# Performance work log

Hardware: AMD Instinct MI355X
Metric: run time of the kernel (lower is better)

## Reference

```python
import jax, jax.numpy as jnp
import numpy as np

ALPHA = 0.25
GAMMA = 2.0
CLS_EPS = 1e-4


def _make_boxes(key, n, img=512.0, smin=32.0, smax=128.0, yx=False):
    k1, k2, k3, k4 = jax.random.split(key, 4)
    cx = jax.random.uniform(k1, (n,)) * img
    cy = jax.random.uniform(k2, (n,)) * img
    w = smin + jax.random.uniform(k3, (n,)) * (smax - smin)
    h = smin + jax.random.uniform(k4, (n,)) * (smax - smin)
    if yx:  # anchor format (y1, x1, y2, x2)
        return jnp.stack([cy - h / 2, cx - w / 2, cy + h / 2, cx + w / 2], axis=1)
    # annotation format (x1, y1, x2, y2)
    return jnp.stack([cx - w / 2, cy - h / 2, cx + w / 2, cy + h / 2], axis=1)


def setup_inputs() -> dict:
    key = jax.random.key(0)
    B, A, C, M = 4, 100000, 80, 32
    k = jax.random.split(key, 6)
    classifications = jax.random.uniform(k[0], (B, A, C), dtype=jnp.float32)
    regressions = jax.random.normal(k[1], (B, A, 7), dtype=jnp.float32)
    anchors = _make_boxes(k[2], A, yx=True)[None]  # [1, A, 4] (y1,x1,y2,x2)
    boxes = jax.vmap(lambda kk: _make_boxes(kk, M))(jax.random.split(k[3], B))  # [B, M, 4]
    labels = jax.random.randint(k[4], (B, M), 0, C).astype(jnp.float32)
    annotations = jnp.concatenate([boxes, labels[..., None]], axis=-1)  # [B, M, 5]
    return {"classifications": classifications, "regressions": regressions,
            "anchors": anchors, "annotations": annotations}


def reference(classifications, regressions, anchors, annotations):
    B, A, C = classifications.shape
    anchor = anchors[0]  # [A, 4] (y1, x1, y2, x2)
    aw = anchor[:, 3] - anchor[:, 1]
    ah = anchor[:, 2] - anchor[:, 0]
    acx = anchor[:, 1] + 0.5 * aw
    acy = anchor[:, 0] + 0.5 * ah
    area_a = (anchor[:, 2] - anchor[:, 0]) * (anchor[:, 3] - anchor[:, 1])

    def per_image(cls, reg, ann):
        M_ = ann.shape[0]
        b = ann[:, :4]  # (x1, y1, x2, y2)
        labels = ann[:, 4].astype(jnp.int32)
        cls = jnp.clip(cls, CLS_EPS, 1.0 - CLS_EPS)
        # IoU [A, M] (same axis convention as calc_iou)
        iw = jnp.clip(jnp.minimum(anchor[:, 3:4], b[None, :, 2]) - jnp.maximum(anchor[:, 1:2], b[None, :, 0]), 0.0)
        ih = jnp.clip(jnp.minimum(anchor[:, 2:3], b[None, :, 3]) - jnp.maximum(anchor[:, 0:1], b[None, :, 1]), 0.0)
        area_b = (b[:, 2] - b[:, 0]) * (b[:, 3] - b[:, 1])
        inter = iw * ih
        ua = jnp.clip(area_a[:, None] + area_b[None, :] - inter, 1e-8)
        iou = inter / ua
        iou_max = iou.max(axis=1)
        iou_argmax = iou.argmax(axis=1)  # [A]
        pos = iou_max >= 0.5
        neg = iou_max < 0.4
        num_pos = pos.sum()
        posf = pos.astype(cls.dtype)
        # classification targets: -1 ignore, 0 background, one-hot positives
        assigned_box = b[iou_argmax]           # [A, 4]
        assigned_lbl = labels[iou_argmax]      # [A]
        onehot = jax.nn.one_hot(assigned_lbl, C, dtype=cls.dtype)
        tgt = jnp.where(pos[:, None], onehot, jnp.where(neg[:, None], 0.0, -1.0))
        alpha_f = jnp.where(tgt == 1.0, ALPHA, 1.0 - ALPHA)
        focal_w = alpha_f * jnp.where(tgt == 1.0, 1.0 - cls, cls) ** GAMMA
        bce = -(tgt * jnp.log(cls) + (1.0 - tgt) * jnp.log(1.0 - cls))
        cls_loss = jnp.where(tgt != -1.0, focal_w * bce, 0.0).sum() / jnp.maximum(num_pos.astype(cls.dtype), 1.0)
        gw = assigned_box[:, 2] - assigned_box[:, 0]
        gh = assigned_box[:, 3] - assigned_box[:, 1]
        gcx = assigned_box[:, 0] + 0.5 * gw
        gcy = assigned_box[:, 1] + 0.5 * gh
        gw = jnp.clip(gw, 1.0)
        gh = jnp.clip(gh, 1.0)
        rt = jnp.stack([(gcy - acy) / ah, (gcx - acx) / aw,
                        jnp.log(gh / ah), jnp.log(gw / aw)], axis=1)  # [A, 4] (dy,dx,dh,dw)
        diff = jnp.abs(rt - reg[:, :4])
        sl1 = jnp.where(diff <= 1.0 / 9.0, 0.5 * 9.0 * diff ** 2, diff - 0.5 / 9.0)
        reg_loss = (sl1 * posf[:, None]).sum() / jnp.maximum(num_pos * 4, 1).astype(cls.dtype)
        # embedding grouping loss (segment mean per GT box over positive anchors)
        emb = reg[:, 4:7]
        counts = jax.ops.segment_sum(posf, iou_argmax, num_segments=M_)          # [M]
        sums = jax.ops.segment_sum(emb * posf[:, None], iou_argmax, num_segments=M_)  # [M, 3]
        mean = jnp.where((counts > 0)[:, None], sums / jnp.maximum(counts, 1.0)[:, None], 0.0)
        mdet = jax.lax.stop_gradient(mean)
        sq = jax.ops.segment_sum((((emb - mdet[iou_argmax]) ** 2).sum(-1)) * posf, iou_argmax, num_segments=M_)
        per_ann = jnp.where(counts > 0, sq / jnp.maximum(counts * 3.0, 1.0), 0.0)
        emb_loss = per_ann.sum() / M_
        return cls_loss, reg_loss, emb_loss, mean

    cls_l, reg_l, emb_l, embs = jax.vmap(per_image)(classifications, regressions, annotations)
    losses = jnp.stack([cls_l.mean(), reg_l.mean() * 50.0, emb_l.mean()])
    return losses, embs
```

## Files before the change

### kernel.cpp

```cpp
#include <hip/hip_runtime.h>

#define CLS_LO 1.0e-4f
#define CLS_HI 0.9999f


__device__ __forceinline__ float smooth_l1(float d) {
    d = fabsf(d);
    return (d <= (1.0f / 9.0f)) ? (4.5f * d * d) : (d - (0.5f / 9.0f));
}

__global__ void __launch_bounds__(256)
det_main_kernel(const float* __restrict__ cls,
                const float* __restrict__ reg,
                const float* __restrict__ anc,
                const float* __restrict__ ann,
                float* __restrict__ ws,
                int A, int C, int M, int NB)
{
    const int b   = blockIdx.y;
    const int tid = threadIdx.x;
    const int a0  = blockIdx.x * 256;
    const int a   = a0 + tid;
    const int S   = 5 * M + 3 * NB;

    __shared__ float sb[5 * 64];
    __shared__ float s_cnt[64], s_sx[64], s_sy[64], s_sz[64], s_sq[64];
    __shared__ float s_maskf[256];

    for (int i = tid; i < M * 5; i += 256)
        sb[i] = ann[(size_t)b * M * 5 + i];
    if (tid < M) { s_cnt[tid] = 0.f; s_sx[tid] = 0.f; s_sy[tid] = 0.f; s_sz[tid] = 0.f; s_sq[tid] = 0.f; }
    s_maskf[tid] = 0.f;
    __syncthreads();

    float contrib_cls = 0.f, contrib_reg = 0.f, contrib_np = 0.f;

    if (a < A) {
        float4 av = ((const float4*)anc)[a];
        const float ay1 = av.x, ax1 = av.y, ay2 = av.z, ax2 = av.w;
        const float aw  = ax2 - ax1;
        const float ah  = ay2 - ay1;
        const float acx = ax1 + 0.5f * aw;
        const float acy = ay1 + 0.5f * ah;
        const float area_a = ah * aw;

        float best = -1.0f;
        int   bj   = 0;
#define IOU_BODY(j)                                                              \
        {                                                                        \
            const float bx1 = sb[(j) * 5 + 0];                                   \
            const float by1 = sb[(j) * 5 + 1];                                   \
            const float bx2 = sb[(j) * 5 + 2];                                   \
            const float by2 = sb[(j) * 5 + 3];                                   \
            float iw = fminf(ax2, bx2) - fmaxf(ax1, bx1); iw = fmaxf(iw, 0.f);   \
            float ih = fminf(ay2, by2) - fmaxf(ay1, by1); ih = fmaxf(ih, 0.f);   \
            const float inter = iw * ih;                                         \
            const float ua = fmaxf(area_a + (bx2 - bx1) * (by2 - by1) - inter,   \
                                   1e-8f);                                       \
            const float iou = inter / ua;                                        \
            if (iou > best) { best = iou; bj = (j); }                            \
        }
        if (M == 32) {
            #pragma unroll
            for (int j = 0; j < 32; j++) IOU_BODY(j)
        } else {
            for (int j = 0; j < M; j++) IOU_BODY(j)
        }
#undef IOU_BODY
        const bool pos = best >= 0.5f;
        const bool neg = best < 0.4f;
        s_maskf[tid] = (pos || neg) ? 1.0f : 0.0f;

        if (pos) {
            contrib_np = 1.0f;

            const float* cbase = cls + ((size_t)b * A + a) * (size_t)C;
            const int L = (int)sb[bj * 5 + 4];
            const float p = fminf(fmaxf(cbase[L], CLS_LO), CLS_HI);
            contrib_cls = 0.25f * (1.f - p) * (1.f - p) * (-__logf(p))
                        - 0.75f * p * p * (-__logf(1.f - p));

            const float* rp = reg + ((size_t)b * A + a) * 7;
            const float r0 = rp[0], r1 = rp[1], r2 = rp[2], r3 = rp[3];
            const float e0 = rp[4], e1 = rp[5], e2 = rp[6];

            const float bx1 = sb[bj * 5 + 0];
            const float by1 = sb[bj * 5 + 1];
            const float bx2 = sb[bj * 5 + 2];
            const float by2 = sb[bj * 5 + 3];
            float gw = bx2 - bx1;
            float gh = by2 - by1;
            const float gcx = bx1 + 0.5f * gw;
            const float gcy = by1 + 0.5f * gh;
            gw = fmaxf(gw, 1.f);
            gh = fmaxf(gh, 1.f);
            contrib_reg = smooth_l1((gcy - acy) / ah - r0) +
                          smooth_l1((gcx - acx) / aw - r1) +
                          smooth_l1(logf(gh / ah) - r2) +
                          smooth_l1(logf(gw / aw) - r3);

            atomicAdd(&s_cnt[bj], 1.f);
            atomicAdd(&s_sx[bj], e0);
            atomicAdd(&s_sy[bj], e1);
            atomicAdd(&s_sz[bj], e2);
            atomicAdd(&s_sq[bj], e0 * e0 + e1 * e1 + e2 * e2);
        }
    }
    __syncthreads();

    {
        const float4* tile = (const float4*)(cls + ((size_t)b * A + a0) * (size_t)C);
        float acc = 0.f;
        if (a0 + 256 <= A && C == 80) {
            #pragma unroll 5
            for (int k = 0; k < 20; k++) {
                const int e4 = tid + 256 * k;
                const float m = s_maskf[(unsigned)e4 / 20u];
                const float4 v = tile[e4];
                float p, l, s = 0.f;
                p = fminf(fmaxf(v.x, CLS_LO), CLS_HI); l = __logf(1.f - p); s = fmaf(p * p, l, s);
                p = fminf(fmaxf(v.y, CLS_LO), CLS_HI); l = __logf(1.f - p); s = fmaf(p * p, l, s);
                p = fminf(fmaxf(v.z, CLS_LO), CLS_HI); l = __logf(1.f - p); s = fmaf(p * p, l, s);
                p = fminf(fmaxf(v.w, CLS_LO), CLS_HI); l = __logf(1.f - p); s = fmaf(p * p, l, s);
                acc = fmaf(m, s, acc);
            }
        } else {
            const int nA   = min(256, A - a0);
            const int cpa4 = C >> 2;
            const int n4   = nA * cpa4;
            for (int e4 = tid; e4 < n4; e4 += 256) {
                const float m = s_maskf[(unsigned)e4 / (unsigned)cpa4];
                const float4 v = tile[e4];
                float p, l, s = 0.f;
                p = fminf(fmaxf(v.x, CLS_LO), CLS_HI); l = __logf(1.f - p); s = fmaf(p * p, l, s);
                p = fminf(fmaxf(v.y, CLS_LO), CLS_HI); l = __logf(1.f - p); s = fmaf(p * p, l, s);
                p = fminf(fmaxf(v.z, CLS_LO), CLS_HI); l = __logf(1.f - p); s = fmaf(p * p, l, s);
                p = fminf(fmaxf(v.w, CLS_LO), CLS_HI); l = __logf(1.f - p); s = fmaf(p * p, l, s);
                acc = fmaf(m, s, acc);
            }
        }
        contrib_cls -= 0.75f * acc;
    }

    for (int off = 32; off > 0; off >>= 1) {
        contrib_cls += __shfl_down(contrib_cls, off, 64);
        contrib_reg += __shfl_down(contrib_reg, off, 64);
        contrib_np  += __shfl_down(contrib_np,  off, 64);
    }
    __shared__ float s_part[4][3];
    if ((tid & 63) == 0) {
        s_part[tid >> 6][0] = contrib_cls;
        s_part[tid >> 6][1] = contrib_reg;
        s_part[tid >> 6][2] = contrib_np;
    }
    __syncthreads();

    float* wsb = ws + (size_t)b * S;
    if (tid < M) {
        const float c = s_cnt[tid];
        if (c != 0.f) {
            atomicAdd(&wsb[tid], c);
            atomicAdd(&wsb[M + 3 * tid + 0], s_sx[tid]);
            atomicAdd(&wsb[M + 3 * tid + 1], s_sy[tid]);
            atomicAdd(&wsb[M + 3 * tid + 2], s_sz[tid]);
            atomicAdd(&wsb[4 * M + tid], s_sq[tid]);
        }
    }
    if (tid == 0) {
        float* slot = wsb + 5 * M + 3 * blockIdx.x;
        slot[0] = s_part[0][0] + s_part[1][0] + s_part[2][0] + s_part[3][0];
        slot[1] = s_part[0][1] + s_part[1][1] + s_part[2][1] + s_part[3][1];
        slot[2] = s_part[0][2] + s_part[1][2] + s_part[2][2] + s_part[3][2];
    }
}

__global__ void __launch_bounds__(256)
det_final_kernel(const float* __restrict__ ws,
                 float* __restrict__ out,
                 int B, int M, int NB)
{
    const int t = threadIdx.x;
    const int S = 5 * M + 3 * NB;
    __shared__ float s_scal[8][3];
    __shared__ float s_emb[8];
    __shared__ float tmp[4][3];
    if (t < B) s_emb[t] = 0.f;

    for (int b = 0; b < B; b++) {
        const float* slots = ws + (size_t)b * S + 5 * M;
        float c = 0.f, r = 0.f, n = 0.f;
        for (int i = t; i < NB; i += 256) {
            c += slots[3 * i + 0];
            r += slots[3 * i + 1];
            n += slots[3 * i + 2];
        }
        for (int off = 32; off > 0; off >>= 1) {
            c += __shfl_down(c, off, 64);
            r += __shfl_down(r, off, 64);
            n += __shfl_down(n, off, 64);
        }
        if ((t & 63) == 0) { tmp[t >> 6][0] = c; tmp[t >> 6][1] = r; tmp[t >> 6][2] = n; }
        __syncthreads();
        if (t == 0) {
            s_scal[b][0] = tmp[0][0] + tmp[1][0] + tmp[2][0] + tmp[3][0];
            s_scal[b][1] = tmp[0][1] + tmp[1][1] + tmp[2][1] + tmp[3][1];
            s_scal[b][2] = tmp[0][2] + tmp[1][2] + tmp[2][2] + tmp[3][2];
        }
        __syncthreads();
    }

    if (t < B * M) {
        const int b = t / M;
        const int m = t - b * M;
        const float* wsb = ws + (size_t)b * S;
        const float c = wsb[m];
        float mx = 0.f, my = 0.f, mz = 0.f, pa = 0.f;
        if (c > 0.f) {
            mx = wsb[M + 3 * m + 0] / c;
            my = wsb[M + 3 * m + 1] / c;
            mz = wsb[M + 3 * m + 2] / c;
            const float sq = wsb[4 * M + m] - c * (mx * mx + my * my + mz * mz);
            pa = sq / fmaxf(c * 3.f, 1.f);
        }
        out[3 + (size_t)(b * M + m) * 3 + 0] = mx;
        out[3 + (size_t)(b * M + m) * 3 + 1] = my;
        out[3 + (size_t)(b * M + m) * 3 + 2] = mz;
        atomicAdd(&s_emb[b], pa);
    }
    __syncthreads();

    if (t == 0) {
        float cl = 0.f, rl = 0.f, el = 0.f;
        for (int b = 0; b < B; b++) {
            const float np = s_scal[b][2];
            cl += s_scal[b][0] / fmaxf(np, 1.f);
            rl += s_scal[b][1] / fmaxf(4.f * np, 1.f);
            el += s_emb[b] / (float)M;
        }
        const float invB = 1.f / (float)B;
        out[0] = cl * invB;
        out[1] = rl * invB * 50.f;
        out[2] = el * invB;
    }
}

extern "C" void kernel_launch(void* const* d_in, const int* in_sizes, int n_in,
                              void* d_out, int out_size, void* d_ws, size_t ws_size,
                              hipStream_t stream) {
    const float* cls = (const float*)d_in[0];
    const float* reg = (const float*)d_in[1];
    const float* anc = (const float*)d_in[2];
    const float* ann = (const float*)d_in[3];
    float* out = (float*)d_out;
    float* ws  = (float*)d_ws;

    const int A = in_sizes[2] / 4;
    const int B = in_sizes[1] / (A * 7);
    const int C = in_sizes[0] / (B * A);
    const int M = in_sizes[3] / (B * 5);
    const int NB = (A + 255) / 256;
    const int S  = 5 * M + 3 * NB;

    hipMemsetAsync(ws, 0, (size_t)B * S * sizeof(float), stream);

    dim3 grid(NB, B);
    det_main_kernel<<<grid, 256, 0, stream>>>(cls, reg, anc, ann, ws, A, C, M, NB);
    det_final_kernel<<<1, 256, 0, stream>>>(ws, out, B, M, NB);
}
```

Measured before the change: 224.9 us.

## Split IoU assignment and focal-loss streaming into separate kernels with byte mask

Splits the fused kernel in two. An assignment kernel computes IoU, writes a per-anchor byte mask to workspace and accumulates the positive-anchor terms. A focal kernel then streams the classification tensor in 64-anchor blocks, using a multiply-shift in place of the division for the mask index. Block partials are now folded into 64 atomic slots per image, so the final reduction is a single wavefront shuffle. This aims to separate the ALU-heavy IoU phase from the bandwidth-bound streaming phase and to raise the block count for the bandwidth phase, at the cost of an extra launch and mask traffic.

```diff
diff --git a/kernel.cpp b/kernel.cpp
--- a/kernel.cpp
+++ b/kernel.cpp
@@ -10,27 +10,30 @@
 }
 
 __global__ void __launch_bounds__(256)
-det_main_kernel(const float* __restrict__ cls,
-                const float* __restrict__ reg,
-                const float* __restrict__ anc,
-                const float* __restrict__ ann,
-                float* __restrict__ ws,
-                int A, int C, int M, int NB)
+det_assign_kernel(const float* __restrict__ cls,
+                  const float* __restrict__ reg,
+                  const float* __restrict__ anc,
+                  const float* __restrict__ ann,
+                  float* __restrict__ ws,
+                  unsigned char* __restrict__ mask,
+                  int A, int C, int M)
 {
     const int b   = blockIdx.y;
     const int tid = threadIdx.x;
-    const int a0  = blockIdx.x * 256;
-    const int a   = a0 + tid;
-    const int S   = 5 * M + 3 * NB;
-
-    __shared__ float sb[5 * 64];
-    __shared__ float s_cnt[64], s_sx[64], s_sy[64], s_sz[64], s_sq[64];
-    __shared__ float s_maskf[256];
-
-    for (int i = tid; i < M * 5; i += 256)
-        sb[i] = ann[(size_t)b * M * 5 + i];
-    if (tid < M) { s_cnt[tid] = 0.f; s_sx[tid] = 0.f; s_sy[tid] = 0.f; s_sz[tid] = 0.f; s_sq[tid] = 0.f; }
-    s_maskf[tid] = 0.f;
+    const int a   = blockIdx.x * 256 + tid;
+    const int S   = 5 * M + 192;
+
+    __shared__ float4 sbox[64];
+    __shared__ float  slbl[64];
+    __shared__ float  s_cnt[64], s_sx[64], s_sy[64], s_sz[64], s_sq[64];
+    __shared__ float  s_part[4][3];
+
+    if (tid < M) {
+        const float* bp = ann + ((size_t)b * M + tid) * 5;
+        sbox[tid] = make_float4(bp[0], bp[1], bp[2], bp[3]);
+        slbl[tid] = bp[4];
+        s_cnt[tid] = 0.f; s_sx[tid] = 0.f; s_sy[tid] = 0.f; s_sz[tid] = 0.f; s_sq[tid] = 0.f;
+    }
     __syncthreads();
 
     float contrib_cls = 0.f, contrib_reg = 0.f, contrib_np = 0.f;
@@ -40,23 +43,18 @@
         const float ay1 = av.x, ax1 = av.y, ay2 = av.z, ax2 = av.w;
         const float aw  = ax2 - ax1;
         const float ah  = ay2 - ay1;
-        const float acx = ax1 + 0.5f * aw;
-        const float acy = ay1 + 0.5f * ah;
         const float area_a = ah * aw;
 
         float best = -1.0f;
         int   bj   = 0;
 #define IOU_BODY(j)                                                              \
         {                                                                        \
-            const float bx1 = sb[(j) * 5 + 0];                                   \
-            const float by1 = sb[(j) * 5 + 1];                                   \
-            const float bx2 = sb[(j) * 5 + 2];                                   \
-            const float by2 = sb[(j) * 5 + 3];                                   \
-            float iw = fminf(ax2, bx2) - fmaxf(ax1, bx1); iw = fmaxf(iw, 0.f);   \
-            float ih = fminf(ay2, by2) - fmaxf(ay1, by1); ih = fmaxf(ih, 0.f);   \
+            const float4 bx = sbox[(j)];                                         \
+            float iw = fminf(ax2, bx.z) - fmaxf(ax1, bx.x); iw = fmaxf(iw, 0.f); \
+            float ih = fminf(ay2, bx.w) - fmaxf(ay1, bx.y); ih = fmaxf(ih, 0.f); \
             const float inter = iw * ih;                                         \
-            const float ua = fmaxf(area_a + (bx2 - bx1) * (by2 - by1) - inter,   \
-                                   1e-8f);                                       \
+            const float ua = fmaxf(area_a + (bx.z - bx.x) * (bx.w - bx.y)        \
+                                   - inter, 1e-8f);                              \
             const float iou = inter / ua;                                        \
             if (iou > best) { best = iou; bj = (j); }                            \
         }
@@ -69,13 +67,13 @@
 #undef IOU_BODY
         const bool pos = best >= 0.5f;
         const bool neg = best < 0.4f;
-        s_maskf[tid] = (pos || neg) ? 1.0f : 0.0f;
+        mask[(size_t)b * A + a] = (pos || neg) ? 1 : 0;
 
         if (pos) {
             contrib_np = 1.0f;
 
             const float* cbase = cls + ((size_t)b * A + a) * (size_t)C;
-            const int L = (int)sb[bj * 5 + 4];
+            const int L = (int)slbl[bj];
             const float p = fminf(fmaxf(cbase[L], CLS_LO), CLS_HI);
             contrib_cls = 0.25f * (1.f - p) * (1.f - p) * (-__logf(p))
                         - 0.75f * p * p * (-__logf(1.f - p));
@@ -84,16 +82,15 @@
             const float r0 = rp[0], r1 = rp[1], r2 = rp[2], r3 = rp[3];
             const float e0 = rp[4], e1 = rp[5], e2 = rp[6];
 
-            const float bx1 = sb[bj * 5 + 0];
-            const float by1 = sb[bj * 5 + 1];
-            const float bx2 = sb[bj * 5 + 2];
-            const float by2 = sb[bj * 5 + 3];
-            float gw = bx2 - bx1;
-            float gh = by2 - by1;
-            const float gcx = bx1 + 0.5f * gw;
-            const float gcy = by1 + 0.5f * gh;
+            const float4 bx = sbox[bj];
+            float gw = bx.z - bx.x;
+            float gh = bx.w - bx.y;
+            const float gcx = bx.x + 0.5f * gw;
+            const float gcy = bx.y + 0.5f * gh;
             gw = fmaxf(gw, 1.f);
             gh = fmaxf(gh, 1.f);
+            const float acx = ax1 + 0.5f * aw;
+            const float acy = ay1 + 0.5f * ah;
             contrib_reg = smooth_l1((gcy - acy) / ah - r0) +
                           smooth_l1((gcx - acx) / aw - r1) +
                           smooth_l1(logf(gh / ah) - r2) +
@@ -106,48 +103,12 @@
             atomicAdd(&s_sq[bj], e0 * e0 + e1 * e1 + e2 * e2);
         }
     }
-    __syncthreads();
-
-    {
-        const float4* tile = (const float4*)(cls + ((size_t)b * A + a0) * (size_t)C);
-        float acc = 0.f;
-        if (a0 + 256 <= A && C == 80) {
-            #pragma unroll 5
-            for (int k = 0; k < 20; k++) {
-                const int e4 = tid + 256 * k;
-                const float m = s_maskf[(unsigned)e4 / 20u];
-                const float4 v = tile[e4];
-                float p, l, s = 0.f;
-                p = fminf(fmaxf(v.x, CLS_LO), CLS_HI); l = __logf(1.f - p); s = fmaf(p * p, l, s);
-                p = fminf(fmaxf(v.y, CLS_LO), CLS_HI); l = __logf(1.f - p); s = fmaf(p * p, l, s);
-                p = fminf(fmaxf(v.z, CLS_LO), CLS_HI); l = __logf(1.f - p); s = fmaf(p * p, l, s);
-                p = fminf(fmaxf(v.w, CLS_LO), CLS_HI); l = __logf(1.f - p); s = fmaf(p * p, l, s);
-                acc = fmaf(m, s, acc);
-            }
-        } else {
-            const int nA   = min(256, A - a0);
-            const int cpa4 = C >> 2;
-            const int n4   = nA * cpa4;
-            for (int e4 = tid; e4 < n4; e4 += 256) {
-                const float m = s_maskf[(unsigned)e4 / (unsigned)cpa4];
-                const float4 v = tile[e4];
-                float p, l, s = 0.f;
-                p = fminf(fmaxf(v.x, CLS_LO), CLS_HI); l = __logf(1.f - p); s = fmaf(p * p, l, s);
-                p = fminf(fmaxf(v.y, CLS_LO), CLS_HI); l = __logf(1.f - p); s = fmaf(p * p, l, s);
-                p = fminf(fmaxf(v.z, CLS_LO), CLS_HI); l = __logf(1.f - p); s = fmaf(p * p, l, s);
-                p = fminf(fmaxf(v.w, CLS_LO), CLS_HI); l = __logf(1.f - p); s = fmaf(p * p, l, s);
-                acc = fmaf(m, s, acc);
-            }
-        }
-        contrib_cls -= 0.75f * acc;
-    }
 
     for (int off = 32; off > 0; off >>= 1) {
         contrib_cls += __shfl_down(contrib_cls, off, 64);
         contrib_reg += __shfl_down(contrib_reg, off, 64);
         contrib_np  += __shfl_down(contrib_np,  off, 64);
     }
-    __shared__ float s_part[4][3];
     if ((tid & 63) == 0) {
         s_part[tid >> 6][0] = contrib_cls;
         s_part[tid >> 6][1] = contrib_reg;
@@ -167,47 +128,101 @@
         }
     }
     if (tid == 0) {
-        float* slot = wsb + 5 * M + 3 * blockIdx.x;
-        slot[0] = s_part[0][0] + s_part[1][0] + s_part[2][0] + s_part[3][0];
-        slot[1] = s_part[0][1] + s_part[1][1] + s_part[2][1] + s_part[3][1];
-        slot[2] = s_part[0][2] + s_part[1][2] + s_part[2][2] + s_part[3][2];
+        const float c = s_part[0][0] + s_part[1][0] + s_part[2][0] + s_part[3][0];
+        const float r = s_part[0][1] + s_part[1][1] + s_part[2][1] + s_part[3][1];
+        const float n = s_part[0][2] + s_part[1][2] + s_part[2][2] + s_part[3][2];
+        float* slot = wsb + 5 * M + 3 * (blockIdx.x & 63);
+        if (c != 0.f) atomicAdd(&slot[0], c);
+        if (r != 0.f) atomicAdd(&slot[1], r);
+        if (n != 0.f) atomicAdd(&slot[2], n);
+    }
+}
+
+template <int CPA4>
+__global__ void __launch_bounds__(256)
+det_focal_kernel(const float* __restrict__ cls,
+                 const unsigned char* __restrict__ mask,
+                 float* __restrict__ ws,
+                 int A, int C, int M)
+{
+    const int b     = blockIdx.y;
+    const int aBase = blockIdx.x * 64;
+    const int tid   = threadIdx.x;
+    const int S     = 5 * M + 192;
+    const int cpa4  = CPA4 ? CPA4 : (C >> 2);
+
+    __shared__ float smask[64];
+    if (tid < 64) {
+        const int a = aBase + tid;
+        smask[tid] = (a < A) ? (float)mask[(size_t)b * A + a] : 0.f;
+    }
+    __syncthreads();
+
+    const int nA = min(64, A - aBase);
+    const float4* tile = (const float4*)(cls + ((size_t)b * A + aBase) * (size_t)C);
+    float acc = 0.f;
+
+#define FOCAL_BODY(IDX, MVAL)                                                     \
+    {                                                                             \
+        const float4 v = tile[(IDX)];                                             \
+        float p, l, s = 0.f;                                                      \
+        p = fminf(fmaxf(v.x, CLS_LO), CLS_HI); l = __logf(1.f - p); s = fmaf(p * p, l, s); \
+        p = fminf(fmaxf(v.y, CLS_LO), CLS_HI); l = __logf(1.f - p); s = fmaf(p * p, l, s); \
+        p = fminf(fmaxf(v.z, CLS_LO), CLS_HI); l = __logf(1.f - p); s = fmaf(p * p, l, s); \
+        p = fminf(fmaxf(v.w, CLS_LO), CLS_HI); l = __logf(1.f - p); s = fmaf(p * p, l, s); \
+        acc = fmaf((MVAL), s, acc);                                               \
+    }
+
+    if (CPA4 == 20 && nA == 64) {
+        #pragma unroll
+        for (int k = 0; k < 5; k++) {
+            const unsigned idx = (unsigned)tid + 256u * k;
+            const float m = smask[(idx * 52429u) >> 20];
+            FOCAL_BODY(idx, m)
+        }
+    } else {
+        const int n4 = nA * cpa4;
+        for (int idx = tid; idx < n4; idx += 256) {
+            const float m = smask[(unsigned)idx / (unsigned)cpa4];
+            FOCAL_BODY(idx, m)
+        }
+    }
+#undef FOCAL_BODY
+
+    for (int off = 32; off > 0; off >>= 1)
+        acc += __shfl_down(acc, off, 64);
+    __shared__ float sp[4];
+    if ((tid & 63) == 0) sp[tid >> 6] = acc;
+    __syncthreads();
+    if (tid == 0) {
+        const float tot = sp[0] + sp[1] + sp[2] + sp[3];
+        atomicAdd(&ws[(size_t)b * S + 5 * M + 3 * (blockIdx.x & 63) + 0], -0.75f * tot);
     }
 }
 
 __global__ void __launch_bounds__(256)
 det_final_kernel(const float* __restrict__ ws,
                  float* __restrict__ out,
-                 int B, int M, int NB)
+                 int B, int M)
 {
     const int t = threadIdx.x;
-    const int S = 5 * M + 3 * NB;
+    const int S = 5 * M + 192;
     __shared__ float s_scal[8][3];
     __shared__ float s_emb[8];
-    __shared__ float tmp[4][3];
     if (t < B) s_emb[t] = 0.f;
 
-    for (int b = 0; b < B; b++) {
-        const float* slots = ws + (size_t)b * S + 5 * M;
-        float c = 0.f, r = 0.f, n = 0.f;
-        for (int i = t; i < NB; i += 256) {
-            c += slots[3 * i + 0];
-            r += slots[3 * i + 1];
-            n += slots[3 * i + 2];
-        }
+    const int k = t & 63;
+    for (int b = t >> 6; b < B; b += 4) {
+        const float* slot = ws + (size_t)b * S + 5 * M + 3 * k;
+        float c = slot[0], r = slot[1], n = slot[2];
         for (int off = 32; off > 0; off >>= 1) {
             c += __shfl_down(c, off, 64);
             r += __shfl_down(r, off, 64);
             n += __shfl_down(n, off, 64);
         }
-        if ((t & 63) == 0) { tmp[t >> 6][0] = c; tmp[t >> 6][1] = r; tmp[t >> 6][2] = n; }
-        __syncthreads();
-        if (t == 0) {
-            s_scal[b][0] = tmp[0][0] + tmp[1][0] + tmp[2][0] + tmp[3][0];
-            s_scal[b][1] = tmp[0][1] + tmp[1][1] + tmp[2][1] + tmp[3][1];
-            s_scal[b][2] = tmp[0][2] + tmp[1][2] + tmp[2][2] + tmp[3][2];
-        }
-        __syncthreads();
-    }
+        if (k == 0) { s_scal[b][0] = c; s_scal[b][1] = r; s_scal[b][2] = n; }
+    }
+    __syncthreads();
 
     if (t < B * M) {
         const int b = t / M;
@@ -258,12 +273,19 @@
     const int B = in_sizes[1] / (A * 7);
     const int C = in_sizes[0] / (B * A);
     const int M = in_sizes[3] / (B * 5);
-    const int NB = (A + 255) / 256;
-    const int S  = 5 * M + 3 * NB;
+    const int S = 5 * M + 192;
+    unsigned char* mask = (unsigned char*)d_ws + (size_t)B * S * sizeof(float);
 
     hipMemsetAsync(ws, 0, (size_t)B * S * sizeof(float), stream);
 
-    dim3 grid(NB, B);
-    det_main_kernel<<<grid, 256, 0, stream>>>(cls, reg, anc, ann, ws, A, C, M, NB);
-    det_final_kernel<<<1, 256, 0, stream>>>(ws, out, B, M, NB);
-}
+    dim3 gridA((A + 255) / 256, B);
+    det_assign_kernel<<<gridA, 256, 0, stream>>>(cls, reg, anc, ann, ws, mask, A, C, M);
+
+    dim3 gridB((A + 63) / 64, B);
+    if (C == 80)
+        det_focal_kernel<20><<<gridB, 256, 0, stream>>>(cls, mask, ws, A, C, M);
+    else
+        det_focal_kernel<0><<<gridB, 256, 0, stream>>>(cls, mask, ws, A, C, M);
+
+    det_final_kernel<<<1, 256, 0, stream>>>(ws, out, B, M);
+}
```

New measurement: 239.0 us. 1.06x slower.
